# Kernel tuning notes

Measured on AMD Instinct MI355X. Metric: run time of the kernel, lower is better.

## Reference

```python
import jax, jax.numpy as jnp
import numpy as np

B, M, FIN = 16, 49152, 16
F1, K = 32, 5
NNZ = 8 * M  # ~8 neighbors per vertex on a HEALPix sphere mesh


def setup_inputs() -> dict:
    key = jax.random.key(0)
    kx, kr, kc, kv, kw, kb = jax.random.split(key, 6)
    x = jax.random.normal(kx, (B, M, FIN), dtype=jnp.float32)
    rows = jax.random.randint(kr, (NNZ,), 0, M, dtype=jnp.int32)
    cols = jax.random.randint(kc, (NNZ,), 0, M, dtype=jnp.int32)
    # small values keep the order-K Chebyshev recurrence numerically tame
    vals = jax.random.normal(kv, (NNZ,), dtype=jnp.float32) * 0.1
    stddev = 1.0 / np.sqrt(FIN * (K + 0.5) / 2.0)
    kernel = jax.random.normal(kw, (FIN * K, F1), dtype=jnp.float32) * stddev
    bias = jax.random.uniform(kb, (1, 1, F1), dtype=jnp.float32) * 0.05
    return {"x": x, "rows": rows, "cols": cols, "vals": vals,
            "kernel": kernel, "bias": bias}


def reference(x, rows, cols, vals, kernel, bias):
    # x: [B, M, Fin]; sparse Laplacian L in COO (rows, cols, vals), shape [M, M]
    b, m, fin = x.shape
    k = kernel.shape[0] // fin

    def spmm(X):  # L @ X for X: [M, Fin*B]
        return jax.ops.segment_sum(vals[:, None] * X[cols], rows, num_segments=m)

    # x0: [M, Fin*B] exactly as the TF transpose/reshape does
    x0 = jnp.transpose(x, (1, 2, 0)).reshape(m, fin * b)
    xs = [x0]
    if k > 1:
        x1 = spmm(x0)
        xs.append(x1)
    for _ in range(2, k):
        x2 = 2.0 * spmm(x1) - x0
        xs.append(x2)
        x0, x1 = x1, x2
    # [K, M, Fin, B] -> [B, M, Fin, K] -> [B*M, Fin*K]
    xk = jnp.stack(xs, axis=0).reshape(k, m, fin, b)
    xk = jnp.transpose(xk, (3, 1, 2, 0)).reshape(b * m, fin * k)
    out = (xk @ kernel).reshape(b, m, -1)  # [B, M, F1]
    return out + bias
```

## Files before the change

kernel.cpp:

```cpp
#include <hip/hip_runtime.h>


constexpr int M   = 49152;
constexpr int B   = 16;
constexpr int FIN = 16;
constexpr int F1  = 32;
constexpr int K   = 5;
constexpr int XBS = M * FIN;
constexpr size_t SLICEB   = (size_t)M * 64;
constexpr size_t BUFBYTES = (size_t)M * 512;
constexpr int NBLK_M = M / 256;
constexpr int NHB = 64 * NBLK_M;

typedef short s16x8 __attribute__((ext_vector_type(8)));
typedef float f32x4 __attribute__((ext_vector_type(4)));
typedef unsigned int u32;
typedef unsigned long long u64;

#define DEVFN __device__ __forceinline__

DEVFN float lo2f(u32 d) {
  union { u32 u; float f; } v; v.u = d << 16; return v.f;
}
DEVFN float hi2f(u32 d) {
  union { u32 u; float f; } v; v.u = d & 0xffff0000u; return v.f;
}
DEVFN unsigned short f2bf(float f) {
  union { float f; u32 u; } v;
  v.f = f;
  u32 r = (v.u + 0x7FFFu + ((v.u >> 16) & 1u)) >> 16;
  return (unsigned short)r;
}


__global__ __launch_bounds__(256) void transform_x(const float* __restrict__ x,
                                                   char* __restrict__ x0b) {
  int lane = threadIdx.x & 63;
  int m = blockIdx.x * 4 + (threadIdx.x >> 6);
  int s = lane >> 3, i = lane & 7;
  int b = 2 * s + (i >> 2), f = (i & 3) * 4;
  float4 v = *(const float4*)(x + (size_t)b * XBS + (size_t)m * FIN + f);
  ushort4 r = make_ushort4(f2bf(v.x), f2bf(v.y), f2bf(v.z), f2bf(v.w));
  *(ushort4*)(x0b + (size_t)s * SLICEB + (size_t)m * 64 + i * 8) = r;
}


__global__ __launch_bounds__(256) void hist_kernel(const int* __restrict__ rows,
                                                   int* __restrict__ counts, int nnz) {
  int i = blockIdx.x * 256 + threadIdx.x;
  if (i < nnz) atomicAdd(&counts[rows[i]], 1);
}

DEVFN int wave_incl_scan(int v, int lane) {
#pragma unroll
  for (int off = 1; off < 64; off <<= 1) {
    int t = __shfl_up(v, off);
    if (lane >= off) v += t;
  }
  return v;
}

__global__ __launch_bounds__(1024) void scan_blocks(const int* __restrict__ src,
                                                    int* __restrict__ dst,
                                                    int* __restrict__ partials) {
  __shared__ int wsum[16];
  int tid = threadIdx.x, lane = tid & 63, w = tid >> 6;
  int i = blockIdx.x * 1024 + tid;
  int s = wave_incl_scan(src[i], lane);
  if (lane == 63) wsum[w] = s;
  __syncthreads();
  if (tid < 16) {
    int t = wsum[tid];
#pragma unroll
    for (int off = 1; off < 16; off <<= 1) {
      int u = __shfl_up(t, off);
      if (tid >= off) t += u;
    }
    wsum[tid] = t;
  }
  __syncthreads();
  int base = (w > 0) ? wsum[w - 1] : 0;
  s += base;
  dst[i + 1] = s;
  if (tid == 1023) partials[blockIdx.x] = s;
}

__global__ void scan_partials_kernel(int* __restrict__ partials,
                                     int* __restrict__ dst, int nblk) {
  int lane = threadIdx.x;
  int v = (lane < nblk) ? partials[lane] : 0;
  v = wave_incl_scan(v, lane);
  if (lane < nblk) partials[lane] = v;
  if (lane == 0) dst[0] = 0;
}

__global__ __launch_bounds__(1024) void scan_add_kernel(int* __restrict__ dst,
                                                        const int* __restrict__ partials) {
  if (blockIdx.x == 0) return;
  int i = blockIdx.x * 1024 + threadIdx.x;
  dst[i + 1] += partials[blockIdx.x - 1];
}

__global__ __launch_bounds__(256) void scatter_kernel(const int* __restrict__ rows,
                                                      const int* __restrict__ cols,
                                                      const float* __restrict__ vals,
                                                      const int* __restrict__ row_ptr,
                                                      int* __restrict__ fill,
                                                      u32* __restrict__ cvp, int nnz) {
  int i = blockIdx.x * 256 + threadIdx.x;
  if (i < nnz) {
    int r = rows[i];
    int pos = row_ptr[r] + atomicAdd(&fill[r], 1);
    cvp[pos] = ((u32)cols[i] << 16) | (u32)f2bf(vals[i]);
  }
}


__global__ __launch_bounds__(256) void deg_hist_blk(const int* __restrict__ counts,
                                                    int* __restrict__ blkhist) {
  __shared__ int lh[64];
  int tid = threadIdx.x;
  if (tid < 64) lh[tid] = 0;
  __syncthreads();
  int m = blockIdx.x * 256 + tid;
  atomicAdd(&lh[min(counts[m], 63)], 1);
  __syncthreads();
  if (tid < 64) blkhist[tid * NBLK_M + blockIdx.x] = lh[tid];
}

__global__ __launch_bounds__(256) void perm_scatter_blk(const int* __restrict__ counts,
                                                        const int* __restrict__ sc,
                                                        int* __restrict__ perm) {
  __shared__ int lh[64];
  __shared__ int lbase[64];
  int tid = threadIdx.x, blk = blockIdx.x;
  if (tid < 64) lh[tid] = 0;
  __syncthreads();
  int m = blk * 256 + tid;
  int d = min(counts[m], 63);
  int lr = atomicAdd(&lh[d], 1);
  __syncthreads();
  if (tid < 64) lbase[tid] = sc[tid * NBLK_M + blk];
  __syncthreads();
  perm[lbase[d] + lr] = m;
}


template <bool SUB>
__global__ __launch_bounds__(256) void spmm_strip(const char* __restrict__ xsrc,
                                                  const char* __restrict__ ssrc,
                                                  char* __restrict__ y,
                                                  const int* __restrict__ row_ptr,
                                                  const int* __restrict__ degs,
                                                  const int* __restrict__ perm,
                                                  const u32* __restrict__ cvp) {
  int s  = blockIdx.x & 7;
  int g4 = blockIdx.x >> 3;
  int lane = threadIdx.x & 63, wave = threadIdx.x >> 6;
  int r = lane >> 3, q = lane & 7;
  int rq = lane & 56;
  int grp = g4 * 4 + wave;
  const char* sbase = xsrc + (size_t)s * SLICEB;
  size_t qb = (size_t)q * 8;

  int rid  = perm[grp * 8 + r];
  int base = row_ptr[rid];
  int deg  = degs[rid];
  int wmax = deg;
  wmax = max(wmax, __shfl_xor(wmax, 8));
  wmax = max(wmax, __shfl_xor(wmax, 16));
  wmax = max(wmax, __shfl_xor(wmax, 32));

  u64 sv = 0;
  if (SUB)
    sv = __builtin_nontemporal_load(
        (const u64*)(ssrc + (size_t)s * SLICEB + (size_t)rid * 64 + qb));

  float a0 = 0.f, a1 = 0.f, a2 = 0.f, a3 = 0.f;
  for (int t0 = 0; t0 < wmax; t0 += 8) {
    int et = t0 + q;
    u32 cvw = 0u;
    if (et < deg) cvw = cvp[base + et];
#pragma unroll
    for (int t = 0; t < 8; ++t) {
      u32 c = (u32)__shfl((int)cvw, rq | t);
      u64 d = *(const u64*)(sbase + (size_t)(c >> 16) * 64 + qb);
      float v = lo2f(c);
      u32 dl = (u32)d, dh = (u32)(d >> 32);
      a0 = fmaf(v, lo2f(dl), a0); a1 = fmaf(v, hi2f(dl), a1);
      a2 = fmaf(v, lo2f(dh), a2); a3 = fmaf(v, hi2f(dh), a3);
    }
  }

  if (SUB) {
    u32 sl = (u32)sv, sh = (u32)(sv >> 32);
    a0 = fmaf(2.f, a0, -lo2f(sl)); a1 = fmaf(2.f, a1, -hi2f(sl));
    a2 = fmaf(2.f, a2, -lo2f(sh)); a3 = fmaf(2.f, a3, -hi2f(sh));
  }
  u64 rv = ((u64)(((u32)f2bf(a3) << 16) | (u32)f2bf(a2)) << 32) |
           (u64)(((u32)f2bf(a1) << 16) | (u32)f2bf(a0));
  __builtin_nontemporal_store(
      rv, (u64*)(y + (size_t)s * SLICEB + (size_t)rid * 64 + qb));
}


__global__ __launch_bounds__(256) void cheb_gemm_mfma(const char* __restrict__ xs0,
                                                      const float* __restrict__ kern,
                                                      const float* __restrict__ bias,
                                                      float* __restrict__ out) {
  __shared__ unsigned short bl[3][4][32][8];
  __shared__ float bsl[32];
  int tid = threadIdx.x;
  for (int idx = tid; idx < 3 * 4 * 32 * 8; idx += 256) {
    int j = idx & 7, o = (idx >> 3) & 31, g = (idx >> 8) & 3, c = idx >> 10;
    int k = 2 * c + (g >> 1), f = (g & 1) * 8 + j;
    bl[c][g][o][j] = (k < K) ? f2bf(kern[(f * K + k) * F1 + o]) : (unsigned short)0;
  }
  if (tid < 32) bsl[tid] = bias[tid];
  __syncthreads();

  int lane = tid & 63;
  int w = blockIdx.x * 4 + (tid >> 6);
  int b = w / 384;
  int mt0 = (w % 384) * 8;

  int row = lane & 15, g = lane >> 4;
  int col = lane & 15;

  s16x8 bf[3][2];
#pragma unroll
  for (int c = 0; c < 3; ++c) {
#pragma unroll
    for (int ot = 0; ot < 2; ++ot)
      bf[c][ot] = *(const s16x8*)(&bl[c][g][col + 16 * ot][0]);
  }
  float bias0 = bsl[col], bias1 = bsl[col + 16];

  size_t lanebyte = (size_t)(b >> 1) * SLICEB + (size_t)row * 64 +
                    (size_t)(b & 1) * 32 + (size_t)(g & 1) * 16;
  int khalf = g >> 1;
  const char* p0 = xs0 + (size_t)(0 + khalf) * BUFBYTES + lanebyte;
  const char* p1 = xs0 + (size_t)(2 + khalf) * BUFBYTES + lanebyte;
  const char* p2 = xs0 + (size_t)(4 + khalf) * BUFBYTES + lanebyte;

  size_t obase0 = ((size_t)b * M + (size_t)mt0 * 16) * F1;

#pragma unroll 2
  for (int t = 0; t < 8; ++t) {
    size_t moff = (size_t)(mt0 + t) * (16 * 64);
    s16x8 a0 = *(const s16x8*)(p0 + moff);
    s16x8 a1 = *(const s16x8*)(p1 + moff);
    s16x8 a2 = (g < 2) ? *(const s16x8*)(p2 + moff) : (s16x8)0;

    f32x4 acc0 = {0.f, 0.f, 0.f, 0.f};
    f32x4 acc1 = {0.f, 0.f, 0.f, 0.f};
    acc0 = __builtin_amdgcn_mfma_f32_16x16x32_bf16(a0, bf[0][0], acc0, 0, 0, 0);
    acc1 = __builtin_amdgcn_mfma_f32_16x16x32_bf16(a0, bf[0][1], acc1, 0, 0, 0);
    acc0 = __builtin_amdgcn_mfma_f32_16x16x32_bf16(a1, bf[1][0], acc0, 0, 0, 0);
    acc1 = __builtin_amdgcn_mfma_f32_16x16x32_bf16(a1, bf[1][1], acc1, 0, 0, 0);
    acc0 = __builtin_amdgcn_mfma_f32_16x16x32_bf16(a2, bf[2][0], acc0, 0, 0, 0);
    acc1 = __builtin_amdgcn_mfma_f32_16x16x32_bf16(a2, bf[2][1], acc1, 0, 0, 0);

    float* ob = out + obase0 + (size_t)t * (16 * F1);
#pragma unroll
    for (int j = 0; j < 4; ++j) {
      int r = g * 4 + j;
      __builtin_nontemporal_store(acc0[j] + bias0, ob + r * F1 + col);
      __builtin_nontemporal_store(acc1[j] + bias1, ob + r * F1 + col + 16);
    }
  }
}


extern "C" void kernel_launch(void* const* d_in, const int* in_sizes, int n_in,
                              void* d_out, int out_size, void* d_ws, size_t ws_size,
                              hipStream_t stream) {
  const float* x    = (const float*)d_in[0];
  const int*   rows = (const int*)d_in[1];
  const int*   cols = (const int*)d_in[2];
  const float* vals = (const float*)d_in[3];
  const float* kern = (const float*)d_in[4];
  const float* bias = (const float*)d_in[5];
  float* out = (float*)d_out;
  int nnz = in_sizes[1];

  char* x0b = (char*)d_ws;
  char* x1b = x0b + BUFBYTES;
  char* x2b = x1b + BUFBYTES;
  char* x3b = x2b + BUFBYTES;
  char* x4b = x3b + BUFBYTES;
  int* row_ptr  = (int*)(x4b + BUFBYTES);
  int* counts   = row_ptr + (M + 256);
  int* fill     = counts + M;
  int* partials = fill + M;
  int* blkhist  = partials + 256;
  int* sc       = blkhist + NHB;
  int* perm     = sc + NHB + 256;
  u32* cvp      = (u32*)(perm + M);

  int nblk1024 = M / 1024;
  int nblkH    = NHB / 1024;
  int nblkNnz  = (nnz + 255) / 256;

  transform_x<<<M / 4, 256, 0, stream>>>(x, x0b);

  hipMemsetAsync(counts, 0, (size_t)2 * M * 4, stream);
  hist_kernel<<<nblkNnz, 256, 0, stream>>>(rows, counts, nnz);
  scan_blocks<<<nblk1024, 1024, 0, stream>>>(counts, row_ptr, partials);
  scan_partials_kernel<<<1, 64, 0, stream>>>(partials, row_ptr, nblk1024);
  scan_add_kernel<<<nblk1024, 1024, 0, stream>>>(row_ptr, partials);
  deg_hist_blk<<<NBLK_M, 256, 0, stream>>>(counts, blkhist);
  scan_blocks<<<nblkH, 1024, 0, stream>>>(blkhist, sc, partials);
  scan_partials_kernel<<<1, 64, 0, stream>>>(partials, sc, nblkH);
  scan_add_kernel<<<nblkH, 1024, 0, stream>>>(sc, partials);
  perm_scatter_blk<<<NBLK_M, 256, 0, stream>>>(counts, sc, perm);
  scatter_kernel<<<nblkNnz, 256, 0, stream>>>(rows, cols, vals, row_ptr, fill, cvp, nnz);

  int spmmGrid = 8 * (M / 32);
  spmm_strip<false><<<spmmGrid, 256, 0, stream>>>(x0b, nullptr, x1b, row_ptr, counts, perm, cvp);
  spmm_strip<true ><<<spmmGrid, 256, 0, stream>>>(x1b, x0b, x2b, row_ptr, counts, perm, cvp);
  spmm_strip<true ><<<spmmGrid, 256, 0, stream>>>(x2b, x1b, x3b, row_ptr, counts, perm, cvp);
  spmm_strip<true ><<<spmmGrid, 256, 0, stream>>>(x3b, x2b, x4b, row_ptr, counts, perm, cvp);

  cheb_gemm_mfma<<<1536, 256, 0, stream>>>(x0b, kern, bias, out);

  (void)n_in; (void)out_size; (void)ws_size; (void)in_sizes;
}
```

Baseline: 286.3 us.

## Process two rows per wave-lane in SpMM and reorder GEMM wave mapping

Each SpMM lane group now handles two rows, issuing all gathers for both rows before the FMAs, with half the grid. This raises memory-level parallelism per wave to hide gather latency, at the cost of more registers and a loop bound that is the max degree of both rows. The GEMM kernel remaps waves so batch pairs sharing a slice are interleaved across neighbouring waves, and switches its output stores from nontemporal to regular.

```diff
diff --git a/kernel.cpp b/kernel.cpp
--- a/kernel.cpp
+++ b/kernel.cpp
@@ -163,44 +163,74 @@
   const char* sbase = xsrc + (size_t)s * SLICEB;
   size_t qb = (size_t)q * 8;
 
-  int rid  = perm[grp * 8 + r];
-  int base = row_ptr[rid];
-  int deg  = degs[rid];
-  int wmax = deg;
+  int ridA = perm[grp * 16 + r];
+  int ridB = perm[grp * 16 + 8 + r];
+  int baseA = row_ptr[ridA], baseB = row_ptr[ridB];
+  int degA = degs[ridA], degB = degs[ridB];
+  int wmax = max(degA, degB);
   wmax = max(wmax, __shfl_xor(wmax, 8));
   wmax = max(wmax, __shfl_xor(wmax, 16));
   wmax = max(wmax, __shfl_xor(wmax, 32));
 
-  u64 sv = 0;
-  if (SUB)
-    sv = __builtin_nontemporal_load(
-        (const u64*)(ssrc + (size_t)s * SLICEB + (size_t)rid * 64 + qb));
-
-  float a0 = 0.f, a1 = 0.f, a2 = 0.f, a3 = 0.f;
+  u64 svA = 0, svB = 0;
+  if (SUB) {
+    svA = __builtin_nontemporal_load(
+        (const u64*)(ssrc + (size_t)s * SLICEB + (size_t)ridA * 64 + qb));
+    svB = __builtin_nontemporal_load(
+        (const u64*)(ssrc + (size_t)s * SLICEB + (size_t)ridB * 64 + qb));
+  }
+
+  float aA0 = 0.f, aA1 = 0.f, aA2 = 0.f, aA3 = 0.f;
+  float aB0 = 0.f, aB1 = 0.f, aB2 = 0.f, aB3 = 0.f;
   for (int t0 = 0; t0 < wmax; t0 += 8) {
     int et = t0 + q;
-    u32 cvw = 0u;
-    if (et < deg) cvw = cvp[base + et];
+    u32 cvA = 0u, cvB = 0u;
+    if (et < degA) cvA = cvp[baseA + et];
+    if (et < degB) cvB = cvp[baseB + et];
+    u32 cA[8], cB[8];
+    u64 dA[8], dB[8];
 #pragma unroll
     for (int t = 0; t < 8; ++t) {
-      u32 c = (u32)__shfl((int)cvw, rq | t);
-      u64 d = *(const u64*)(sbase + (size_t)(c >> 16) * 64 + qb);
-      float v = lo2f(c);
-      u32 dl = (u32)d, dh = (u32)(d >> 32);
-      a0 = fmaf(v, lo2f(dl), a0); a1 = fmaf(v, hi2f(dl), a1);
-      a2 = fmaf(v, lo2f(dh), a2); a3 = fmaf(v, hi2f(dh), a3);
+      cA[t] = (u32)__shfl((int)cvA, rq | t);
+      dA[t] = *(const u64*)(sbase + (size_t)(cA[t] >> 16) * 64 + qb);
+    }
+#pragma unroll
+    for (int t = 0; t < 8; ++t) {
+      cB[t] = (u32)__shfl((int)cvB, rq | t);
+      dB[t] = *(const u64*)(sbase + (size_t)(cB[t] >> 16) * 64 + qb);
+    }
+#pragma unroll
+    for (int t = 0; t < 8; ++t) {
+      float v = lo2f(cA[t]);
+      u32 dl = (u32)dA[t], dh = (u32)(dA[t] >> 32);
+      aA0 = fmaf(v, lo2f(dl), aA0); aA1 = fmaf(v, hi2f(dl), aA1);
+      aA2 = fmaf(v, lo2f(dh), aA2); aA3 = fmaf(v, hi2f(dh), aA3);
+    }
+#pragma unroll
+    for (int t = 0; t < 8; ++t) {
+      float v = lo2f(cB[t]);
+      u32 dl = (u32)dB[t], dh = (u32)(dB[t] >> 32);
+      aB0 = fmaf(v, lo2f(dl), aB0); aB1 = fmaf(v, hi2f(dl), aB1);
+      aB2 = fmaf(v, lo2f(dh), aB2); aB3 = fmaf(v, hi2f(dh), aB3);
     }
   }
 
   if (SUB) {
-    u32 sl = (u32)sv, sh = (u32)(sv >> 32);
-    a0 = fmaf(2.f, a0, -lo2f(sl)); a1 = fmaf(2.f, a1, -hi2f(sl));
-    a2 = fmaf(2.f, a2, -lo2f(sh)); a3 = fmaf(2.f, a3, -hi2f(sh));
-  }
-  u64 rv = ((u64)(((u32)f2bf(a3) << 16) | (u32)f2bf(a2)) << 32) |
-           (u64)(((u32)f2bf(a1) << 16) | (u32)f2bf(a0));
+    u32 sl = (u32)svA, sh = (u32)(svA >> 32);
+    aA0 = fmaf(2.f, aA0, -lo2f(sl)); aA1 = fmaf(2.f, aA1, -hi2f(sl));
+    aA2 = fmaf(2.f, aA2, -lo2f(sh)); aA3 = fmaf(2.f, aA3, -hi2f(sh));
+    sl = (u32)svB; sh = (u32)(svB >> 32);
+    aB0 = fmaf(2.f, aB0, -lo2f(sl)); aB1 = fmaf(2.f, aB1, -hi2f(sl));
+    aB2 = fmaf(2.f, aB2, -lo2f(sh)); aB3 = fmaf(2.f, aB3, -hi2f(sh));
+  }
+  u64 rvA = ((u64)(((u32)f2bf(aA3) << 16) | (u32)f2bf(aA2)) << 32) |
+            (u64)(((u32)f2bf(aA1) << 16) | (u32)f2bf(aA0));
+  u64 rvB = ((u64)(((u32)f2bf(aB3) << 16) | (u32)f2bf(aB2)) << 32) |
+            (u64)(((u32)f2bf(aB1) << 16) | (u32)f2bf(aB0));
   __builtin_nontemporal_store(
-      rv, (u64*)(y + (size_t)s * SLICEB + (size_t)rid * 64 + qb));
+      rvA, (u64*)(y + (size_t)s * SLICEB + (size_t)ridA * 64 + qb));
+  __builtin_nontemporal_store(
+      rvB, (u64*)(y + (size_t)s * SLICEB + (size_t)ridB * 64 + qb));
 }
 
 
@@ -221,8 +251,9 @@
 
   int lane = tid & 63;
   int w = blockIdx.x * 4 + (tid >> 6);
-  int b = w / 384;
-  int mt0 = (w % 384) * 8;
+  int bb = w & 1, pair = (w >> 1) & 7, mtg = w >> 4;
+  int b = pair * 2 + bb;
+  int mt0 = mtg * 8;
 
   int row = lane & 15, g = lane >> 4;
   int col = lane & 15;
@@ -236,8 +267,8 @@
   }
   float bias0 = bsl[col], bias1 = bsl[col + 16];
 
-  size_t lanebyte = (size_t)(b >> 1) * SLICEB + (size_t)row * 64 +
-                    (size_t)(b & 1) * 32 + (size_t)(g & 1) * 16;
+  size_t lanebyte = (size_t)pair * SLICEB + (size_t)row * 64 +
+                    (size_t)bb * 32 + (size_t)(g & 1) * 16;
   int khalf = g >> 1;
   const char* p0 = xs0 + (size_t)(0 + khalf) * BUFBYTES + lanebyte;
   const char* p1 = xs0 + (size_t)(2 + khalf) * BUFBYTES + lanebyte;
@@ -265,8 +296,8 @@
 #pragma unroll
     for (int j = 0; j < 4; ++j) {
       int r = g * 4 + j;
-      __builtin_nontemporal_store(acc0[j] + bias0, ob + r * F1 + col);
-      __builtin_nontemporal_store(acc1[j] + bias1, ob + r * F1 + col + 16);
+      ob[r * F1 + col]      = acc0[j] + bias0;
+      ob[r * F1 + col + 16] = acc1[j] + bias1;
     }
   }
 }
@@ -316,7 +347,7 @@
   perm_scatter_blk<<<NBLK_M, 256, 0, stream>>>(counts, sc, perm);
   scatter_kernel<<<nblkNnz, 256, 0, stream>>>(rows, cols, vals, row_ptr, fill, cvp, nnz);
 
-  int spmmGrid = 8 * (M / 32);
+  int spmmGrid = 8 * (M / 64);
   spmm_strip<false><<<spmmGrid, 256, 0, stream>>>(x0b, nullptr, x1b, row_ptr, counts, perm, cvp);
   spmm_strip<true ><<<spmmGrid, 256, 0, stream>>>(x1b, x0b, x2b, row_ptr, counts, perm, cvp);
   spmm_strip<true ><<<spmmGrid, 256, 0, stream>>>(x2b, x1b, x3b, row_ptr, counts, perm, cvp);
```

Result: no change. 287.1 us (+0.3%).
